# Kernel optimization log

Measured on AMD Instinct MI355X. Metric: run time of the kernel, lower is better.

## Reference

```python
import jax, jax.numpy as jnp
import numpy as np

B, S, H = 4, 2048, 1024
NH = 16
DH = H // NH  # 64


def setup_inputs() -> dict:
    key = jax.random.key(0)
    ks = jax.random.split(key, 11)
    s = 1.0 / np.sqrt(H)
    inp = {
        "key": jax.random.normal(ks[0], (B, S, H), jnp.float32),
        "value": jax.random.normal(ks[1], (B, S, H), jnp.float32),
        "query": jax.random.normal(ks[2], (B, S, H), jnp.float32),
        # linear_layers[0] -> applied to query, [1] -> key, [2] -> value
        "wq": jax.random.normal(ks[3], (H, H), jnp.float32) * s,
        "bq": jnp.zeros((H,), jnp.float32),
        "wk": jax.random.normal(ks[4], (H, H), jnp.float32) * s,
        "bk": jnp.zeros((H,), jnp.float32),
        "wv": jax.random.normal(ks[5], (H, H), jnp.float32) * s,
        "bv": jnp.zeros((H,), jnp.float32),
        "wo": jax.random.normal(ks[6], (H, H), jnp.float32) * s,
        "bo": jnp.zeros((H,), jnp.float32),
    }
    return inp


def reference(key, value, query, wq, bq, wk, bk, wv, bv, wo, bo):
    # QKV projections; split heads -> [B, NH, S, DH]
    def proj(x, w, b):
        y = jnp.einsum("bsh,hd->bsd", x, w) + b
        return y.reshape(B, S, NH, DH).transpose(0, 2, 1, 3)

    q = proj(query, wq, bq)
    k = proj(key, wk, bk)
    v = proj(value, wv, bv)

    scores = jnp.einsum("bnqd,bnkd->bnqk", q, k) / jnp.sqrt(jnp.float32(DH))
    probs = jax.nn.softmax(scores, axis=-1)  # dropout p=0 -> identity
    out = jnp.einsum("bnqk,bnkd->bnqd", probs, v)
    out = out.transpose(0, 2, 1, 3).reshape(B, S, H)
    return jnp.einsum("bsh,hd->bsd", out, wo) + bo
```

## Files before the change

kernel.cpp:

```cpp
#include <hip/hip_runtime.h>
#include <hip/hip_bf16.h>

constexpr int kB = 4, kS = 2048, kH = 1024, kNH = 16, kDH = 64;
constexpr int kM = kB * kS;

typedef short short8 __attribute__((ext_vector_type(8)));
typedef float f32x4 __attribute__((ext_vector_type(4)));
typedef float f32x16 __attribute__((ext_vector_type(16)));

__device__ inline unsigned int pack2bf16(float lo, float hi) {
  __hip_bfloat162 h;
  h.x = __float2bfloat16(lo);
  h.y = __float2bfloat16(hi);
  unsigned int u;
  __builtin_memcpy(&u, &h, 4);
  return u;
}

__device__ inline void gload_lds16(const unsigned short* g, unsigned short* l) {
  auto* gp = (const __attribute__((address_space(1))) unsigned int*)(uintptr_t)g;
  auto* lp = (__attribute__((address_space(3))) unsigned int*)(unsigned int)(uintptr_t)l;
  __builtin_amdgcn_global_load_lds(gp, lp, 16, 0, 0);
}

__global__ __launch_bounds__(256) void f32_to_bf16_vec3(
    const float* __restrict__ i0, const float* __restrict__ i1,
    const float* __restrict__ i2, __hip_bfloat16* __restrict__ o0,
    __hip_bfloat16* __restrict__ o1, __hip_bfloat16* __restrict__ o2) {
  const int z = blockIdx.y;
  const float* in = z == 0 ? i0 : z == 1 ? i1 : i2;
  __hip_bfloat16* out = z == 0 ? o0 : z == 1 ? o1 : o2;
  const int i = blockIdx.x * 256 + threadIdx.x;
  const float4 v = ((const float4*)in)[i];
  union { __hip_bfloat16 h[4]; uint2 u; } p;
  p.h[0] = __float2bfloat16(v.x);
  p.h[1] = __float2bfloat16(v.y);
  p.h[2] = __float2bfloat16(v.z);
  p.h[3] = __float2bfloat16(v.w);
  ((uint2*)out)[i] = p.u;
}

__global__ __launch_bounds__(256) void transpose4_f32_to_bf16(
    const float* __restrict__ w0, const float* __restrict__ w1,
    const float* __restrict__ w2, const float* __restrict__ w3,
    __hip_bfloat16* __restrict__ o0, __hip_bfloat16* __restrict__ o1,
    __hip_bfloat16* __restrict__ o2, __hip_bfloat16* __restrict__ o3) {
  const int z = blockIdx.z;
  const float* in = z == 0 ? w0 : z == 1 ? w1 : z == 2 ? w2 : w3;
  __hip_bfloat16* out = z == 0 ? o0 : z == 1 ? o1 : z == 2 ? o2 : o3;
  constexpr int R = kH, C = kH;
  __shared__ float t[32][33];
  const int r0 = blockIdx.y * 32, c0 = blockIdx.x * 32;
  const int tx = threadIdx.x, ty = threadIdx.y;
#pragma unroll
  for (int i = 0; i < 32; i += 8)
    t[ty + i][tx] = in[(size_t)(r0 + ty + i) * C + c0 + tx];
  __syncthreads();
#pragma unroll
  for (int i = 0; i < 32; i += 8)
    out[(size_t)(c0 + ty + i) * R + r0 + tx] = __float2bfloat16(t[tx][ty + i]);
}

__global__ __launch_bounds__(256, 4) void gemm_qkv(
    const unsigned short* __restrict__ A0, const unsigned short* __restrict__ A1,
    const unsigned short* __restrict__ A2, const unsigned short* __restrict__ W0,
    const unsigned short* __restrict__ W1, const unsigned short* __restrict__ W2,
    const float* __restrict__ b0, const float* __restrict__ b1,
    const float* __restrict__ b2, unsigned short* __restrict__ O0,
    unsigned short* __restrict__ O1, unsigned short* __restrict__ O2) {
  constexpr int K = kH;
  __shared__ unsigned short sA[2][128 * 32];
  __shared__ unsigned short sB[2][128 * 32];
  const int tid = threadIdx.x;
  const int wave = tid >> 6, lane = tid & 63;
  const int n16 = lane & 15, quad = lane >> 4;

  const int hw = blockIdx.x + (blockIdx.y << 3) + ((int)blockIdx.z << 9);
  const int wid = (hw & 7) * 192 + (hw >> 3);
  const int z = wid >> 9;
  const int rem = wid & 511;
  const int n0 = (rem & 7) * 128, m0 = (rem >> 3) * 128;

  const unsigned short* A = z == 0 ? A0 : z == 1 ? A1 : A2;
  const unsigned short* W = z == 0 ? W0 : z == 1 ? W1 : W2;
  const float* bias = z == 0 ? b0 : z == 1 ? b1 : b2;

  const int rh = (wave >> 1) * 64, ch = (wave & 1) * 64;
  const int srow = 32 * wave + (lane >> 2);
  const int sk = (lane & 3) * 8;
  const unsigned short* gA = A + (size_t)(m0 + srow) * K + sk;
  const unsigned short* gB = W + (size_t)(n0 + srow) * K + sk;

  const f32x4 zero4 = {0.f, 0.f, 0.f, 0.f};
  f32x4 acc[4][4];
#pragma unroll
  for (int i = 0; i < 4; ++i)
#pragma unroll
    for (int j = 0; j < 4; ++j) acc[i][j] = zero4;

#pragma unroll
  for (int j = 0; j < 2; ++j) {
    gload_lds16(gA + (size_t)(16 * j) * K, &sA[0][(32 * wave + 16 * j) * 32]);
    gload_lds16(gB + (size_t)(16 * j) * K, &sB[0][(32 * wave + 16 * j) * 32]);
  }
  __syncthreads();

  int cur = 0;
  for (int k0 = 0; k0 < K; k0 += 32) {
    const int kn = (k0 + 32 < K) ? k0 + 32 : 0;
#pragma unroll
    for (int j = 0; j < 2; ++j) {
      gload_lds16(gA + (size_t)(16 * j) * K + kn,
                  &sA[cur ^ 1][(32 * wave + 16 * j) * 32]);
      gload_lds16(gB + (size_t)(16 * j) * K + kn,
                  &sB[cur ^ 1][(32 * wave + 16 * j) * 32]);
    }

    short8 af[4], bfr[4];
#pragma unroll
    for (int i = 0; i < 4; ++i)
      af[i] = *(const short8*)&sA[cur][(rh + i * 16 + n16) * 32 + quad * 8];
#pragma unroll
    for (int i = 0; i < 4; ++i)
      bfr[i] = *(const short8*)&sB[cur][(ch + i * 16 + n16) * 32 + quad * 8];
#pragma unroll
    for (int mi = 0; mi < 4; ++mi)
#pragma unroll
      for (int ni = 0; ni < 4; ++ni)
        acc[mi][ni] = __builtin_amdgcn_mfma_f32_16x16x32_bf16(
            af[mi], bfr[ni], acc[mi][ni], 0, 0, 0);

    __syncthreads();
    cur ^= 1;
  }

  __hip_bfloat16* Obf = (__hip_bfloat16*)(z == 0 ? O0 : z == 1 ? O1 : O2);
  const float osc = z == 0 ? 0.18033688011112042f : 1.0f;
#pragma unroll
  for (int ni = 0; ni < 4; ++ni) {
    const int n = n0 + ch + ni * 16 + n16;
    const float bv = bias[n];
    const int hh = n >> 6, dd = n & 63;
#pragma unroll
    for (int mi = 0; mi < 4; ++mi) {
      const int mbase = m0 + rh + mi * 16 + quad * 4;
      const int bb = mbase >> 11, ss = mbase & 2047;
      if (z == 2) {
        const size_t idx = ((size_t)(bb * kNH + hh) * kDH + dd) * kS + ss;
        uint2 w;
        w.x = pack2bf16(acc[mi][ni][0] + bv, acc[mi][ni][1] + bv);
        w.y = pack2bf16(acc[mi][ni][2] + bv, acc[mi][ni][3] + bv);
        *(uint2*)&Obf[idx] = w;
      } else {
        const size_t base = ((size_t)(bb * kNH + hh) * kS + ss) * kDH + dd;
#pragma unroll
        for (int r = 0; r < 4; ++r)
          Obf[base + (size_t)r * kDH] =
              __float2bfloat16((acc[mi][ni][r] + bv) * osc);
      }
    }
  }
}

__global__ __launch_bounds__(256) void gemm_out(
    const unsigned short* __restrict__ A, const unsigned short* __restrict__ Bt,
    const float* __restrict__ bias, float* __restrict__ C, int M, int N, int K) {
  __shared__ unsigned short sA[2][128 * 32];
  __shared__ unsigned short sB[2][128 * 32];
  const int tid = threadIdx.x;
  const int wave = tid >> 6, lane = tid & 63;
  const int n16 = lane & 15, quad = lane >> 4;

  const int hw = blockIdx.x + blockIdx.y * gridDim.x;
  const int cpx = (gridDim.x * gridDim.y) >> 3;
  const int wid = (hw & 7) * cpx + (hw >> 3);
  const int n0 = (wid % gridDim.x) * 128, m0 = (wid / gridDim.x) * 128;

  const int rh = (wave >> 1) * 64, ch = (wave & 1) * 64;
  const int srow = 32 * wave + (lane >> 2);
  const int sk = (lane & 3) * 8;
  const unsigned short* gA = A + (size_t)(m0 + srow) * K + sk;
  const unsigned short* gB = Bt + (size_t)(n0 + srow) * K + sk;

  const f32x4 zero4 = {0.f, 0.f, 0.f, 0.f};
  f32x4 acc[4][4];
#pragma unroll
  for (int i = 0; i < 4; ++i)
#pragma unroll
    for (int j = 0; j < 4; ++j) acc[i][j] = zero4;

#pragma unroll
  for (int j = 0; j < 2; ++j) {
    gload_lds16(gA + (size_t)(16 * j) * K, &sA[0][(32 * wave + 16 * j) * 32]);
    gload_lds16(gB + (size_t)(16 * j) * K, &sB[0][(32 * wave + 16 * j) * 32]);
  }
  __syncthreads();

  int cur = 0;
  for (int k0 = 0; k0 < K; k0 += 32) {
    const int kn = (k0 + 32 < K) ? k0 + 32 : 0;
#pragma unroll
    for (int j = 0; j < 2; ++j) {
      gload_lds16(gA + (size_t)(16 * j) * K + kn,
                  &sA[cur ^ 1][(32 * wave + 16 * j) * 32]);
      gload_lds16(gB + (size_t)(16 * j) * K + kn,
                  &sB[cur ^ 1][(32 * wave + 16 * j) * 32]);
    }

    short8 af[4], bfr[4];
#pragma unroll
    for (int i = 0; i < 4; ++i)
      af[i] = *(const short8*)&sA[cur][(rh + i * 16 + n16) * 32 + quad * 8];
#pragma unroll
    for (int i = 0; i < 4; ++i)
      bfr[i] = *(const short8*)&sB[cur][(ch + i * 16 + n16) * 32 + quad * 8];
#pragma unroll
    for (int mi = 0; mi < 4; ++mi)
#pragma unroll
      for (int ni = 0; ni < 4; ++ni)
        acc[mi][ni] = __builtin_amdgcn_mfma_f32_16x16x32_bf16(
            af[mi], bfr[ni], acc[mi][ni], 0, 0, 0);

    __syncthreads();
    cur ^= 1;
  }

#pragma unroll
  for (int ni = 0; ni < 4; ++ni) {
    const int n = n0 + ch + ni * 16 + n16;
    const float bv = bias[n];
#pragma unroll
    for (int mi = 0; mi < 4; ++mi) {
#pragma unroll
      for (int r = 0; r < 4; ++r) {
        const int m = m0 + rh + mi * 16 + quad * 4 + r;
        C[(size_t)m * N + n] = acc[mi][ni][r] + bv;
      }
    }
  }
}

__global__ __launch_bounds__(256) void attn_mfma(
    const unsigned short* __restrict__ Q, const unsigned short* __restrict__ K,
    const unsigned short* __restrict__ V, __hip_bfloat16* __restrict__ ctx) {
  __shared__ unsigned short sK[64][72];
  __shared__ unsigned short sVT[64][72];

  const int tid = threadIdx.x;
  const int wave = tid >> 6, lane = tid & 63;
  const int l31 = lane & 31, hi = lane >> 5;

  const int hw = blockIdx.x + ((int)blockIdx.y << 4);
  const int wid = (hw & 7) * 128 + (hw >> 3);
  const int bh = wid >> 4;
  const int q0 = (wid & 15) * 128;

  const unsigned short* Qb = Q + (size_t)bh * (kS * kDH);
  const unsigned short* Kb = K + (size_t)bh * (kS * kDH);
  const unsigned short* Vb = V + (size_t)bh * (kS * kDH);

  const int qrow = q0 + wave * 32 + l31;
  short8 qf[4];
#pragma unroll
  for (int c = 0; c < 4; ++c)
    qf[c] = *(const short8*)(Qb + (size_t)qrow * kDH + c * 16 + hi * 8);

  float l_part = 0.f;
  f32x16 oacc[2];
#pragma unroll
  for (int db = 0; db < 2; ++db)
#pragma unroll
    for (int i = 0; i < 16; ++i) oacc[db][i] = 0.f;

  const int srow = tid >> 2, scol = (tid & 3) * 16;

  uint4 ka, kb2, va, vb;
  auto loadtile = [&](int kk) {
    ka = *(const uint4*)(Kb + (size_t)(kk + srow) * kDH + scol);
    kb2 = *(const uint4*)(Kb + (size_t)(kk + srow) * kDH + scol + 8);
    va = *(const uint4*)(Vb + (size_t)srow * kS + kk + scol);
    vb = *(const uint4*)(Vb + (size_t)srow * kS + kk + scol + 8);
  };
  auto writetile = [&]() {
    *(uint4*)&sK[srow][scol] = ka;
    *(uint4*)&sK[srow][scol + 8] = kb2;
    *(uint4*)&sVT[srow][scol] = va;
    *(uint4*)&sVT[srow][scol + 8] = vb;
  };

  loadtile(0);
  writetile();
  __syncthreads();

  for (int k0 = 0; k0 < kS; k0 += 64) {
    const int kn = (k0 + 64 < kS) ? k0 + 64 : 0;
    loadtile(kn);

    short8 pfrag[4];
#pragma unroll
    for (int kbi = 0; kbi < 2; ++kbi) {
      f32x16 sacc;
#pragma unroll
      for (int i = 0; i < 16; ++i) sacc[i] = 0.f;
      __builtin_amdgcn_s_setprio(1);
#pragma unroll
      for (int c = 0; c < 4; ++c) {
        const short8 af = *(const short8*)&sK[kbi * 32 + l31][c * 16 + hi * 8];
        sacc = __builtin_amdgcn_mfma_f32_32x32x16_bf16(af, qf[c], sacc, 0, 0, 0);
      }
      __builtin_amdgcn_s_setprio(0);

      unsigned int w[8];
#pragma unroll
      for (int m = 0; m < 8; ++m) {
        const float p0 = __builtin_amdgcn_exp2f(sacc[2 * m]);
        const float p1 = __builtin_amdgcn_exp2f(sacc[2 * m + 1]);
        l_part += p0 + p1;
        w[m] = pack2bf16(p0, p1);
      }
      asm("v_permlane32_swap_b32 %0, %1" : "+v"(w[0]), "+v"(w[2]));
      asm("v_permlane32_swap_b32 %0, %1" : "+v"(w[1]), "+v"(w[3]));
      asm("v_permlane32_swap_b32 %0, %1" : "+v"(w[4]), "+v"(w[6]));
      asm("v_permlane32_swap_b32 %0, %1" : "+v"(w[5]), "+v"(w[7]));
      union { unsigned int u[4]; short8 s; } f0, f1;
      f0.u[0] = w[0]; f0.u[1] = w[1]; f0.u[2] = w[2]; f0.u[3] = w[3];
      f1.u[0] = w[4]; f1.u[1] = w[5]; f1.u[2] = w[6]; f1.u[3] = w[7];
      pfrag[kbi * 2] = f0.s;
      pfrag[kbi * 2 + 1] = f1.s;
    }

    __builtin_amdgcn_s_setprio(1);
#pragma unroll
    for (int t = 0; t < 4; ++t) {
#pragma unroll
      for (int db = 0; db < 2; ++db) {
        const short8 vf = *(const short8*)&sVT[db * 32 + l31][t * 16 + hi * 8];
        oacc[db] = __builtin_amdgcn_mfma_f32_32x32x16_bf16(vf, pfrag[t],
                                                           oacc[db], 0, 0, 0);
      }
    }
    __builtin_amdgcn_s_setprio(0);

    __syncthreads();
    writetile();
    __syncthreads();
  }

  const float l = l_part + __shfl_xor(l_part, 32);
  const float inv = 1.f / l;

  const int bb = bh >> 4, hh = bh & 15;
  __hip_bfloat16* dst = ctx + ((size_t)(bb * kS + qrow)) * kH + hh * kDH;
#pragma unroll
  for (int db = 0; db < 2; ++db) {
#pragma unroll
    for (int g = 0; g < 4; ++g) {
      uint2 w;
      w.x = pack2bf16(oacc[db][4 * g] * inv, oacc[db][4 * g + 1] * inv);
      w.y = pack2bf16(oacc[db][4 * g + 2] * inv, oacc[db][4 * g + 3] * inv);
      *(uint2*)(dst + db * 32 + g * 8 + hi * 4) = w;
    }
  }
}

extern "C" void kernel_launch(void* const* d_in, const int* in_sizes, int n_in,
                              void* d_out, int out_size, void* d_ws, size_t ws_size,
                              hipStream_t stream) {
  const float* key   = (const float*)d_in[0];
  const float* value = (const float*)d_in[1];
  const float* query = (const float*)d_in[2];
  const float* wq = (const float*)d_in[3];
  const float* bq = (const float*)d_in[4];
  const float* wk = (const float*)d_in[5];
  const float* bk = (const float*)d_in[6];
  const float* wv = (const float*)d_in[7];
  const float* bv = (const float*)d_in[8];
  const float* wo = (const float*)d_in[9];
  const float* bo = (const float*)d_in[10];
  float* out = (float*)d_out;

  const size_t SZ = (size_t)kB * kS * kH;
  unsigned short* p = (unsigned short*)d_ws;
  unsigned short* actb = p; p += SZ;
  unsigned short* Qh   = p; p += SZ;
  unsigned short* Kh   = p; p += SZ;
  unsigned short* Vh   = p; p += SZ;
  unsigned short* ctxh = p; p += SZ;
  unsigned short* wqt  = p; p += (size_t)kH * kH;
  unsigned short* wkt  = p; p += (size_t)kH * kH;
  unsigned short* wvt  = p; p += (size_t)kH * kH;
  unsigned short* wot  = p; p += (size_t)kH * kH;
  unsigned short* actk = ctxh;
  unsigned short* actv = (unsigned short*)out;

  const dim3 tb(32, 8);
  const dim3 tg(kH / 32, kH / 32, 4);
  transpose4_f32_to_bf16<<<tg, tb, 0, stream>>>(
      wq, wk, wv, wo, (__hip_bfloat16*)wqt, (__hip_bfloat16*)wkt,
      (__hip_bfloat16*)wvt, (__hip_bfloat16*)wot);

  const int cvblocks = (int)(SZ / 4 / 256);
  f32_to_bf16_vec3<<<dim3(cvblocks, 3), 256, 0, stream>>>(
      query, key, value, (__hip_bfloat16*)actb, (__hip_bfloat16*)actk,
      (__hip_bfloat16*)actv);

  gemm_qkv<<<dim3(kH / 128, kM / 128, 3), 256, 0, stream>>>(
      actb, actk, actv, wqt, wkt, wvt, bq, bk, bv, Qh, Kh, Vh);

  dim3 ga(kS / 128, kB * kNH);
  attn_mfma<<<ga, 256, 0, stream>>>(Qh, Kh, Vh, (__hip_bfloat16*)ctxh);

  dim3 gg(kH / 128, kM / 128);
  gemm_out<<<gg, 256, 0, stream>>>(ctxh, wot, bo, out, kM, kH, kH);
}
```

Baseline: 369.2 us.

## Process two query groups per wave to reuse K/V LDS fragments in attention

Each wave now handles 64 query rows, as two 32-row groups, instead of 32, so a block covers 256 queries and the grid halves. K fragments loaded from LDS are reused across both query groups, and V fragments feed two MFMA accumulations. This halves the K/V tile loads from global memory and LDS per query. The cost is doubled accumulator and Q register state and fewer blocks, which could lower occupancy. The launch_bounds occupancy hint of 2 is meant to limit that.

```diff
diff --git a/kernel.cpp b/kernel.cpp
--- a/kernel.cpp
+++ b/kernel.cpp
@@ -240,7 +240,7 @@
   }
 }
 
-__global__ __launch_bounds__(256) void attn_mfma(
+__global__ __launch_bounds__(256, 2) void attn_mfma(
     const unsigned short* __restrict__ Q, const unsigned short* __restrict__ K,
     const unsigned short* __restrict__ V, __hip_bfloat16* __restrict__ ctx) {
   __shared__ unsigned short sK[64][72];
@@ -250,27 +250,32 @@
   const int wave = tid >> 6, lane = tid & 63;
   const int l31 = lane & 31, hi = lane >> 5;
 
-  const int hw = blockIdx.x + ((int)blockIdx.y << 4);
-  const int wid = (hw & 7) * 128 + (hw >> 3);
-  const int bh = wid >> 4;
-  const int q0 = (wid & 15) * 128;
+  const int hw = blockIdx.x + ((int)blockIdx.y << 3);
+  const int wid = (hw & 7) * 64 + (hw >> 3);
+  const int bh = wid >> 3;
+  const int q0 = (wid & 7) * 256;
 
   const unsigned short* Qb = Q + (size_t)bh * (kS * kDH);
   const unsigned short* Kb = K + (size_t)bh * (kS * kDH);
   const unsigned short* Vb = V + (size_t)bh * (kS * kDH);
 
-  const int qrow = q0 + wave * 32 + l31;
-  short8 qf[4];
-#pragma unroll
-  for (int c = 0; c < 4; ++c)
-    qf[c] = *(const short8*)(Qb + (size_t)qrow * kDH + c * 16 + hi * 8);
-
-  float l_part = 0.f;
-  f32x16 oacc[2];
-#pragma unroll
-  for (int db = 0; db < 2; ++db)
-#pragma unroll
-    for (int i = 0; i < 16; ++i) oacc[db][i] = 0.f;
+  const int qbase = q0 + wave * 64;
+  short8 qf[2][4];
+#pragma unroll
+  for (int g = 0; g < 2; ++g)
+#pragma unroll
+    for (int c = 0; c < 4; ++c)
+      qf[g][c] = *(const short8*)(Qb + (size_t)(qbase + g * 32 + l31) * kDH +
+                                  c * 16 + hi * 8);
+
+  float l_part0 = 0.f, l_part1 = 0.f;
+  f32x16 oacc[2][2];
+#pragma unroll
+  for (int g = 0; g < 2; ++g)
+#pragma unroll
+    for (int db = 0; db < 2; ++db)
+#pragma unroll
+      for (int i = 0; i < 16; ++i) oacc[g][db][i] = 0.f;
 
   const int srow = tid >> 2, scol = (tid & 3) * 16;
 
@@ -296,37 +301,45 @@
     const int kn = (k0 + 64 < kS) ? k0 + 64 : 0;
     loadtile(kn);
 
-    short8 pfrag[4];
+    short8 pfrag[2][4];
 #pragma unroll
     for (int kbi = 0; kbi < 2; ++kbi) {
-      f32x16 sacc;
-#pragma unroll
-      for (int i = 0; i < 16; ++i) sacc[i] = 0.f;
-      __builtin_amdgcn_s_setprio(1);
-#pragma unroll
-      for (int c = 0; c < 4; ++c) {
-        const short8 af = *(const short8*)&sK[kbi * 32 + l31][c * 16 + hi * 8];
-        sacc = __builtin_amdgcn_mfma_f32_32x32x16_bf16(af, qf[c], sacc, 0, 0, 0);
+      short8 af[4];
+#pragma unroll
+      for (int c = 0; c < 4; ++c)
+        af[c] = *(const short8*)&sK[kbi * 32 + l31][c * 16 + hi * 8];
+#pragma unroll
+      for (int g = 0; g < 2; ++g) {
+        f32x16 sacc;
+#pragma unroll
+        for (int i = 0; i < 16; ++i) sacc[i] = 0.f;
+        __builtin_amdgcn_s_setprio(1);
+#pragma unroll
+        for (int c = 0; c < 4; ++c)
+          sacc = __builtin_amdgcn_mfma_f32_32x32x16_bf16(af[c], qf[g][c],
+                                                         sacc, 0, 0, 0);
+        __builtin_amdgcn_s_setprio(0);
+
+        unsigned int w[8];
+        float lp = 0.f;
+#pragma unroll
+        for (int m = 0; m < 8; ++m) {
+          const float p0 = __builtin_amdgcn_exp2f(sacc[2 * m]);
+          const float p1 = __builtin_amdgcn_exp2f(sacc[2 * m + 1]);
+          lp += p0 + p1;
+          w[m] = pack2bf16(p0, p1);
+        }
+        if (g == 0) l_part0 += lp; else l_part1 += lp;
+        asm("v_permlane32_swap_b32 %0, %1" : "+v"(w[0]), "+v"(w[2]));
+        asm("v_permlane32_swap_b32 %0, %1" : "+v"(w[1]), "+v"(w[3]));
+        asm("v_permlane32_swap_b32 %0, %1" : "+v"(w[4]), "+v"(w[6]));
+        asm("v_permlane32_swap_b32 %0, %1" : "+v"(w[5]), "+v"(w[7]));
+        union { unsigned int u[4]; short8 s; } f0, f1;
+        f0.u[0] = w[0]; f0.u[1] = w[1]; f0.u[2] = w[2]; f0.u[3] = w[3];
+        f1.u[0] = w[4]; f1.u[1] = w[5]; f1.u[2] = w[6]; f1.u[3] = w[7];
+        pfrag[g][kbi * 2] = f0.s;
+        pfrag[g][kbi * 2 + 1] = f1.s;
       }
-      __builtin_amdgcn_s_setprio(0);
-
-      unsigned int w[8];
-#pragma unroll
-      for (int m = 0; m < 8; ++m) {
-        const float p0 = __builtin_amdgcn_exp2f(sacc[2 * m]);
-        const float p1 = __builtin_amdgcn_exp2f(sacc[2 * m + 1]);
-        l_part += p0 + p1;
-        w[m] = pack2bf16(p0, p1);
-      }
-      asm("v_permlane32_swap_b32 %0, %1" : "+v"(w[0]), "+v"(w[2]));
-      asm("v_permlane32_swap_b32 %0, %1" : "+v"(w[1]), "+v"(w[3]));
-      asm("v_permlane32_swap_b32 %0, %1" : "+v"(w[4]), "+v"(w[6]));
-      asm("v_permlane32_swap_b32 %0, %1" : "+v"(w[5]), "+v"(w[7]));
-      union { unsigned int u[4]; short8 s; } f0, f1;
-      f0.u[0] = w[0]; f0.u[1] = w[1]; f0.u[2] = w[2]; f0.u[3] = w[3];
-      f1.u[0] = w[4]; f1.u[1] = w[5]; f1.u[2] = w[6]; f1.u[3] = w[7];
-      pfrag[kbi * 2] = f0.s;
-      pfrag[kbi * 2 + 1] = f1.s;
     }
 
     __builtin_amdgcn_s_setprio(1);
@@ -335,8 +348,10 @@
 #pragma unroll
       for (int db = 0; db < 2; ++db) {
         const short8 vf = *(const short8*)&sVT[db * 32 + l31][t * 16 + hi * 8];
-        oacc[db] = __builtin_amdgcn_mfma_f32_32x32x16_bf16(vf, pfrag[t],
-                                                           oacc[db], 0, 0, 0);
+        oacc[0][db] = __builtin_amdgcn_mfma_f32_32x32x16_bf16(vf, pfrag[0][t],
+                                                              oacc[0][db], 0, 0, 0);
+        oacc[1][db] = __builtin_amdgcn_mfma_f32_32x32x16_bf16(vf, pfrag[1][t],
+                                                              oacc[1][db], 0, 0, 0);
       }
     }
     __builtin_amdgcn_s_setprio(0);
@@ -346,19 +361,26 @@
     __syncthreads();
   }
 
-  const float l = l_part + __shfl_xor(l_part, 32);
-  const float inv = 1.f / l;
+  const float l0 = l_part0 + __shfl_xor(l_part0, 32);
+  const float l1 = l_part1 + __shfl_xor(l_part1, 32);
+  const float inv[2] = {1.f / l0, 1.f / l1};
 
   const int bb = bh >> 4, hh = bh & 15;
-  __hip_bfloat16* dst = ctx + ((size_t)(bb * kS + qrow)) * kH + hh * kDH;
-#pragma unroll
-  for (int db = 0; db < 2; ++db) {
-#pragma unroll
-    for (int g = 0; g < 4; ++g) {
-      uint2 w;
-      w.x = pack2bf16(oacc[db][4 * g] * inv, oacc[db][4 * g + 1] * inv);
-      w.y = pack2bf16(oacc[db][4 * g + 2] * inv, oacc[db][4 * g + 3] * inv);
-      *(uint2*)(dst + db * 32 + g * 8 + hi * 4) = w;
+#pragma unroll
+  for (int g = 0; g < 2; ++g) {
+    const int qrow = qbase + g * 32 + l31;
+    __hip_bfloat16* dst = ctx + ((size_t)(bb * kS + qrow)) * kH + hh * kDH;
+#pragma unroll
+    for (int db = 0; db < 2; ++db) {
+#pragma unroll
+      for (int gr = 0; gr < 4; ++gr) {
+        uint2 w;
+        w.x = pack2bf16(oacc[g][db][4 * gr] * inv[g],
+                        oacc[g][db][4 * gr + 1] * inv[g]);
+        w.y = pack2bf16(oacc[g][db][4 * gr + 2] * inv[g],
+                        oacc[g][db][4 * gr + 3] * inv[g]);
+        *(uint2*)(dst + db * 32 + gr * 8 + hi * 4) = w;
+      }
     }
   }
 }
@@ -407,7 +429,7 @@
   gemm_qkv<<<dim3(kH / 128, kM / 128, 3), 256, 0, stream>>>(
       actb, actk, actv, wqt, wkt, wvt, bq, bk, bv, Qh, Kh, Vh);
 
-  dim3 ga(kS / 128, kB * kNH);
+  dim3 ga(kS / 256, kB * kNH);
   attn_mfma<<<ga, 256, 0, stream>>>(Qh, Kh, Vh, (__hip_bfloat16*)ctxh);
 
   dim3 gg(kH / 128, kM / 128);
```

After: 338.0 us. -8.4%, faster.
